# Performance work log

Measured on AMD Instinct MI355X. Metric: run time of the kernel, lower is better.

Reference implementation:

```python
import jax, jax.numpy as jnp
import numpy as np

N, M, K = 4, 50, 240000
POS_THRESH = 0.7
NEG_THRESH = 0.3
RPN_BATCH = 512
NUM_FG = RPN_BATCH // 2
NUM_BG = RPN_BATCH - NUM_FG
NEG_INF = -1e9


def setup_inputs() -> dict:
    key = jax.random.key(0)
    k1, k2, k3, k4, k5, k6 = jax.random.split(key, 6)
    # anchors: valid boxes (x1,y1,x2,y2) inside a ~960x600 image
    a_xy = jax.random.uniform(k1, (K, 2)) * jnp.array([900.0, 550.0])
    a_wh = jax.random.uniform(k2, (K, 2)) * 120.0 + 16.0
    anchors = jnp.concatenate([a_xy, a_xy + a_wh], axis=-1)
    g_xy = jax.random.uniform(k3, (N, M, 2)) * jnp.array([900.0, 550.0])
    g_wh = jax.random.uniform(k4, (N, M, 2)) * 120.0 + 16.0
    gt_boxes = jnp.concatenate([g_xy, g_xy + g_wh], axis=-1)
    rpn_cls_score = jax.random.normal(k5, (N, K))
    gt_labels = jax.random.randint(k6, (N, M), 1, 3, dtype=jnp.int32)
    return {"anchors": anchors, "rpn_cls_score": rpn_cls_score,
            "gt_boxes": gt_boxes, "gt_labels": gt_labels}


def _iou(anchors, gt_boxes):
    # anchors (K,4), gt_boxes (N,M,4) -> (N,K,M)
    a = anchors[None, :, None, :]   # (1,K,1,4)
    g = gt_boxes[:, None, :, :]     # (N,1,M,4)
    lt = jnp.maximum(a[..., :2], g[..., :2])
    rb = jnp.minimum(a[..., 2:], g[..., 2:])
    wh = jnp.clip(rb - lt, 0.0)
    inter = wh[..., 0] * wh[..., 1]
    area_a = (a[..., 2] - a[..., 0]) * (a[..., 3] - a[..., 1])
    area_g = (g[..., 2] - g[..., 0]) * (g[..., 3] - g[..., 1])
    return inter / (area_a + area_g - inter + 1e-8)


def _encode(anchors, matched):
    # anchors (K,4), matched (N,K,4) -> (N,K,4) standard (dx,dy,dw,dh)
    aw = anchors[:, 2] - anchors[:, 0]
    ah = anchors[:, 3] - anchors[:, 1]
    acx = anchors[:, 0] + 0.5 * aw
    acy = anchors[:, 1] + 0.5 * ah
    gw = matched[..., 2] - matched[..., 0]
    gh = matched[..., 3] - matched[..., 1]
    gcx = matched[..., 0] + 0.5 * gw
    gcy = matched[..., 1] + 0.5 * gh
    return jnp.stack([(gcx - acx) / aw, (gcy - acy) / ah,
                      jnp.log(gw / aw), jnp.log(gh / ah)], axis=-1)


def _subsample_one(score, pos, neg):
    # deterministic balanced sampler: top NUM_FG positives and top NUM_BG
    # negatives ranked by objectness criterion (hard mining)
    pos_key = jnp.where(pos, score, NEG_INF)
    neg_key = jnp.where(neg, score, NEG_INF)
    pv, pi = jax.lax.top_k(pos_key, NUM_FG)
    nv, ni = jax.lax.top_k(neg_key, NUM_BG)
    mask = jnp.zeros(score.shape[0], dtype=score.dtype)
    mask = mask.at[pi].max((pv > NEG_INF / 2).astype(score.dtype))
    mask = mask.at[ni].max((nv > NEG_INF / 2).astype(score.dtype))
    return mask


def reference(anchors, rpn_cls_score, gt_boxes, gt_labels):
    ious = _iou(anchors, gt_boxes)                 # (N,K,M)
    max_o = jnp.max(ious, axis=-1)                 # (N,K)
    argm = jnp.argmax(ious, axis=-1)               # (N,K)
    pos = max_o >= POS_THRESH
    neg = max_o < NEG_THRESH
    matched = jnp.take_along_axis(
        gt_boxes, jnp.broadcast_to(argm[:, :, None], (N, K, 4)), axis=1)
    matched_labels = jnp.take_along_axis(gt_labels, argm, axis=1)
    cls_targets = jnp.where(pos, matched_labels, 0)
    reg_targets = _encode(anchors, matched) * pos[..., None].astype(anchors.dtype)
    cls_weights = (pos | neg).astype(anchors.dtype)
    reg_weights = pos.astype(anchors.dtype)
    mask = jax.vmap(_subsample_one)(rpn_cls_score, pos, neg)  # (N,K)
    cls_weights = cls_weights * mask
    reg_weights = reg_weights * mask
    return cls_targets, reg_targets, cls_weights, reg_weights
```

## Files before the change

kernel.cpp:

```cpp
#include <hip/hip_runtime.h>

#define KA 240000
#define NI 4
#define MG 50
#define NSEL 256u
#define CAPL 4096
#define BPI 235
#define GRID (BPI * NI)
#define BPIK 469
#define GRIDK (BPIK * NI)

typedef unsigned int u32;

#define METAO 16384
#define LISTO (METAO + 32)
#define ONE_F 0x3F800000u

static __device__ __forceinline__ u32 sortkey32(float f) {
    u32 b = __float_as_uint(f);
    return (b & 0x80000000u) ? ~b : (b | 0x80000000u);
}
static __device__ __forceinline__ void patch1(u32* p) {
    __hip_atomic_store(p, ONE_F, __ATOMIC_RELAXED, __HIP_MEMORY_SCOPE_AGENT);
}

extern "C" __global__ void __launch_bounds__(256, 8)
AnchorTargetLayer_48052094107725_kernel(
    const float4* __restrict__ anchors, const float* __restrict__ scores,
    const float4* __restrict__ gtb, const int* __restrict__ glab,
    float* __restrict__ out, u32* __restrict__ flags, u32* __restrict__ ws) {
#pragma clang fp contract(off)
    __shared__ float4 gA[MG];
    __shared__ float gar[MG];
    __shared__ int glb[MG];
    __shared__ u32 lh[2048];
    const int bx = blockIdx.x;
    const int tid = threadIdx.x;
    const int n = bx / BPIK;
    const int kb = bx - n * BPIK;

    if (tid < 9) {
        const int i = bx * 9 + tid;
        if (i < LISTO) atomicExch(&ws[i], 0u);
    }
    for (int i = tid; i < 2048; i += 256) lh[i] = 0;
    if (tid < MG) {
        const float4 G = gtb[n * MG + tid];
        gA[tid] = G;
        gar[tid] = (G.z - G.x) * (G.w - G.y);
        glb[tid] = glab[n * MG + tid];
    }
    __syncthreads();

    const int k0 = (kb * 256 + tid) * 2;
    if (k0 < KA) {
        float ax0[2], ay0[2], ax2[2], ay2[2];
        #pragma unroll
        for (int j = 0; j < 2; ++j) {
            const float4 A = anchors[k0 + j];
            ax0[j] = A.x; ay0[j] = A.y; ax2[j] = A.z; ay2[j] = A.w;
        }
        float aaw[2], aah[2], aar[2];
        float biE[2], bSE[2], biO[2], bSO[2];
        int bixE[2], bixO[2];
        #pragma unroll
        for (int j = 0; j < 2; ++j) {
            aaw[j] = ax2[j] - ax0[j];
            aah[j] = ay2[j] - ay0[j];
            aar[j] = aaw[j] * aah[j];
            biE[j] = -1.0f; bSE[j] = 1.0f; bixE[j] = 0;
            biO[j] = -1.0f; bSO[j] = 1.0f; bixO[j] = 1;
        }
        #pragma unroll 5
        for (int m = 0; m < MG; m += 2) {
            const float4 Ga = gA[m];
            const float4 Gb = gA[m + 1];
            const float gaA = gar[m];
            const float gaB = gar[m + 1];
            #pragma unroll
            for (int j = 0; j < 2; ++j) {
                const float wa = fmaxf(fminf(ax2[j], Ga.z) - fmaxf(ax0[j], Ga.x), 0.0f);
                const float ha = fmaxf(fminf(ay2[j], Ga.w) - fmaxf(ay0[j], Ga.y), 0.0f);
                const float ia = wa * ha;
                const float sa = aar[j] + gaA;
                if (ia * bSE[j] > biE[j] * sa) { biE[j] = ia; bSE[j] = sa; bixE[j] = m; }
                const float wb = fmaxf(fminf(ax2[j], Gb.z) - fmaxf(ax0[j], Gb.x), 0.0f);
                const float hb = fmaxf(fminf(ay2[j], Gb.w) - fmaxf(ay0[j], Gb.y), 0.0f);
                const float ib = wb * hb;
                const float sb = aar[j] + gaB;
                if (ib * bSO[j] > biO[j] * sb) { biO[j] = ib; bSO[j] = sb; bixO[j] = m + 1; }
            }
        }

        const int nk = n * KA + k0;
        const float2 s2 = ((const float2*)scores)[nk >> 1];
        const float scv[2] = {s2.x, s2.y};

        float clsv[2];
        float4 regv[2];
        u32 flagpack = 0;
        #pragma unroll
        for (int j = 0; j < 2; ++j) {
            const float pO = biO[j] * bSE[j];
            const float pE = biE[j] * bSO[j];
            const bool takeO = (pO > pE) || (pO == pE && bixO[j] < bixE[j]);
            const float bi = takeO ? biO[j] : biE[j];
            const int  bix = takeO ? bixO[j] : bixE[j];
            const float da = ((aar[j] + gar[bix]) - bi) + 1e-8f;
            const float q = bi / da;
            const bool pos = q >= 0.7f;
            const bool neg = q < 0.3f;
            clsv[j] = pos ? (float)glb[bix] : 0.0f;
            float4 rv = make_float4(0.0f, 0.0f, 0.0f, 0.0f);
            if (pos) {
                const float4 Gm = gA[bix];
                const float gw = Gm.z - Gm.x, gh = Gm.w - Gm.y;
                const float gcx = Gm.x + 0.5f * gw, gcy = Gm.y + 0.5f * gh;
                const float acx = ax0[j] + 0.5f * aaw[j], acy = ay0[j] + 0.5f * aah[j];
                rv.x = (gcx - acx) / aaw[j];
                rv.y = (gcy - acy) / aah[j];
                rv.z = logf(gw / aaw[j]);
                rv.w = logf(gh / aah[j]);
            }
            regv[j] = rv;
            const u32 fl = pos ? 1u : (neg ? 2u : 0u);
            flagpack |= fl << (8 * j);
            if (fl) atomicAdd(&lh[sortkey32(scv[j]) >> 21], fl == 2u ? 0x10000u : 1u);
        }
        const size_t NK = (size_t)NI * KA;
        const int t2 = nk >> 1;
        ((float2*)out)[t2] = make_float2(clsv[0], clsv[1]);
        float4* regp = ((float4*)(out + NK)) + nk;
        regp[0] = regv[0]; regp[1] = regv[1];
        const float2 z2 = make_float2(0.0f, 0.0f);
        ((float2*)out)[(5 * NK >> 1) + t2] = z2;
        ((float2*)out)[(6 * NK >> 1) + t2] = z2;
        ((unsigned short*)flags)[t2] = (unsigned short)flagpack;
    }
    __syncthreads();
    const int gp = 2 * n;
    for (int i = tid; i < 2048; i += 256) {
        const u32 c = lh[i];
        if (c & 0xFFFFu) atomicAdd(&ws[gp * 2048 + i], c & 0xFFFFu);
        if (c >> 16)     atomicAdd(&ws[(gp + 1) * 2048 + i], c >> 16);
    }
}

__global__ void __launch_bounds__(256) kP(const float* __restrict__ scores,
                                          const u32* __restrict__ flagsW,
                                          u32* __restrict__ ws,
                                          float* __restrict__ out) {
    __shared__ u32 wsum[4];
    __shared__ u32 s_us[2], s_R[2], s_done[2];
    const int bx = blockIdx.x, tid = threadIdx.x;
    const int n = bx / BPI, kb = bx - n * BPI;
    const int lane = tid & 63, wv = tid >> 6;
    u32* hist = ws;
    u32* meta = ws + METAO;
    u32* list = ws + LISTO;

    for (int gi = 0; gi < 2; ++gi) {
        const int g = 2 * n + gi;
        u32 loc[8];
        u32 s = 0;
        const int base = g * 2048 + tid * 8;
        #pragma unroll
        for (int j = 0; j < 8; ++j) { loc[j] = hist[base + j]; s += loc[j]; }
        u32 v = s;
        #pragma unroll
        for (int d = 1; d < 64; d <<= 1) {
            const u32 t = __shfl_down(v, (unsigned)d, 64);
            v += (lane + d < 64) ? t : 0u;
        }
        if (lane == 0) wsum[wv] = v;
        __syncthreads();
        const u32 t0 = wsum[0], t1 = wsum[1], t2 = wsum[2], t3 = wsum[3];
        const u32 tot = t0 + t1 + t2 + t3;
        u32 above = 0;
        if (wv == 0) above = t1 + t2 + t3;
        else if (wv == 1) above = t2 + t3;
        else if (wv == 2) above = t3;
        v += above;
        if (tid == 0) s_done[gi] = (tot < NSEL) ? 1u : 0u;
        u32 run = v - s;
        #pragma unroll
        for (int j = 7; j >= 0; --j) {
            const u32 Sj = run + loc[j];
            if (Sj >= NSEL && run < NSEL) {
                s_us[gi] = (u32)(tid * 8 + j);
                s_R[gi] = NSEL - run;
            }
            run = Sj;
        }
        __syncthreads();
    }
    if (kb == 0 && tid == 0) {
        meta[2 * n] = s_us[0];     meta[8 + 2 * n] = s_R[0];     meta[16 + 2 * n] = s_done[0];
        meta[2 * n + 1] = s_us[1]; meta[8 + 2 * n + 1] = s_R[1]; meta[16 + 2 * n + 1] = s_done[1];
    }

    const int k0 = (kb * 256 + tid) * 4;
    if (k0 >= KA) return;
    const int nk = n * KA + k0;
    const u32 fw = flagsW[nk >> 2];
    if (!fw) return;
    const float4 s4 = ((const float4*)scores)[nk >> 2];
    const float scv[4] = {s4.x, s4.y, s4.z, s4.w};
    const size_t NK = (size_t)NI * KA;
    u32* o32 = (u32*)out;
    #pragma unroll
    for (int j = 0; j < 4; ++j) {
        const u32 f = (fw >> (8 * j)) & 255u;
        if (!f) continue;
        const int gi = (f == 2u) ? 1 : 0;
        bool in = false;
        if (s_done[gi]) {
            in = true;
        } else {
            const u32 key = sortkey32(scv[j]);
            const u32 p11 = key >> 21;
            if (p11 > s_us[gi]) {
                in = true;
            } else if (p11 == s_us[gi]) {
                const int g = 2 * n + gi;
                const u32 p = atomicAdd(&meta[24 + g], 1u);
                if (p < CAPL) {
                    list[(g * CAPL + p) * 2] = key;
                    list[(g * CAPL + p) * 2 + 1] = (u32)(k0 + j);
                }
            }
        }
        if (in) {
            patch1(&o32[5 * NK + nk + j]);
            if (f == 1u) patch1(&o32[6 * NK + nk + j]);
        }
    }
}

__global__ void __launch_bounds__(256) kR2(const u32* __restrict__ ws,
                                           float* __restrict__ out) {
    __shared__ u32 h2[1024];
    __shared__ u32 cs[256];
    __shared__ u32 s_usb, s_R2, s_tc;
    __shared__ u32 tk[256], ti[256];
    const u32* meta = ws + METAO;
    const u32* list = ws + LISTO;
    const int g = blockIdx.x, tid = threadIdx.x;
    if (meta[16 + g]) return;
    u32 c = meta[24 + g];
    if (c > CAPL) c = CAPL;
    const u32 R1 = meta[8 + g];
    for (u32 i = tid; i < 1024; i += 256) h2[i] = 0;
    if (tid == 0) s_tc = 0;
    __syncthreads();
    for (u32 j = tid; j < c; j += 256)
        atomicAdd(&h2[(list[(g * CAPL + j) * 2] >> 11) & 1023u], 1u);
    __syncthreads();
    u32 loc[4];
    u32 s = 0;
    #pragma unroll
    for (int j = 0; j < 4; ++j) { loc[j] = h2[tid * 4 + j]; s += loc[j]; }
    cs[tid] = s;
    __syncthreads();
    for (int d = 1; d < 256; d <<= 1) {
        const u32 add = (tid + d < 256) ? cs[tid + d] : 0u;
        __syncthreads();
        cs[tid] += add;
        __syncthreads();
    }
    u32 run = (tid < 255) ? cs[tid + 1] : 0u;
    #pragma unroll
    for (int j = 3; j >= 0; --j) {
        const u32 Sj = run + loc[j];
        if (Sj >= R1 && run < R1) { s_usb = (u32)(tid * 4 + j); s_R2 = R1 - run; }
        run = Sj;
    }
    __syncthreads();
    const u32 usb = s_usb, R2 = s_R2;
    const int nn = g >> 1;
    const bool posg = ((g & 1) == 0);
    const size_t NK = (size_t)NI * KA;
    u32* o32 = (u32*)out;
    for (u32 j = tid; j < c; j += 256) {
        const u32 key = list[(g * CAPL + j) * 2];
        const u32 idx = list[(g * CAPL + j) * 2 + 1];
        const u32 sb = (key >> 11) & 1023u;
        if (sb > usb) {
            const size_t o = (size_t)nn * KA + idx;
            patch1(&o32[5 * NK + o]);
            if (posg) patch1(&o32[6 * NK + o]);
        } else if (sb == usb) {
            const u32 p = atomicAdd(&s_tc, 1u);
            if (p < 256) { tk[p] = key; ti[p] = idx; }
        }
    }
    __syncthreads();
    u32 tc = s_tc;
    if (tc > 256) tc = 256;
    for (u32 i = tid; i < tc; i += 256) {
        const u32 ki = tk[i], ii = ti[i];
        u32 rank = 0;
        for (u32 j = 0; j < tc; ++j) {
            const u32 kj = tk[j];
            if (kj > ki || (kj == ki && ti[j] < ii)) rank++;
        }
        if (rank < R2) {
            const size_t o = (size_t)nn * KA + ii;
            patch1(&o32[5 * NK + o]);
            if (posg) patch1(&o32[6 * NK + o]);
        }
    }
}

extern "C" void kernel_launch(void* const* d_in, const int* in_sizes, int n_in,
                              void* d_out, int out_size, void* d_ws, size_t ws_size,
                              hipStream_t stream) {
    (void)in_sizes; (void)n_in; (void)out_size; (void)ws_size;
    const float4* anchors = (const float4*)d_in[0];
    const float*  scores  = (const float*)d_in[1];
    const float4* gtb     = (const float4*)d_in[2];
    const int*    glab    = (const int*)d_in[3];
    float* out = (float*)d_out;

    u32* ws = (u32*)d_ws;
    u32* flags = ws + LISTO + 8 * CAPL * 2;

    AnchorTargetLayer_48052094107725_kernel<<<GRIDK, 256, 0, stream>>>(
        anchors, scores, gtb, glab, out, flags, ws);
    kP<<<GRID, 256, 0, stream>>>(scores, flags, ws, out);
    kR2<<<8, 256, 0, stream>>>(ws, out);
}
```

Before: 126.0 us.

## Fuse final refinement pass into kP via last-block-done arrival counter

Removes the separate kR2 launch. Each kP block now bumps a per-image arrival counter after draining its memory writes, and the last block for an image runs the second-level radix refinement for both the positive and negative groups. This saves one kernel launch and its gap, but the refinement for each image now runs serially in a single block, and correctness depends on the counter being reset and on the atomic visibility ordering.

```diff
diff --git a/kernel.cpp b/kernel.cpp
--- a/kernel.cpp
+++ b/kernel.cpp
@@ -13,7 +13,8 @@
 typedef unsigned int u32;
 
 #define METAO 16384
-#define LISTO (METAO + 32)
+#define ARRO  (METAO + 32)
+#define LISTO (METAO + 40)
 #define ONE_F 0x3F800000u
 
 static __device__ __forceinline__ u32 sortkey32(float f) {
@@ -22,6 +23,15 @@
 }
 static __device__ __forceinline__ void patch1(u32* p) {
     __hip_atomic_store(p, ONE_F, __ATOMIC_RELAXED, __HIP_MEMORY_SCOPE_AGENT);
+}
+static __device__ __forceinline__ void astore(u32* p, u32 v) {
+    __hip_atomic_store(p, v, __ATOMIC_RELAXED, __HIP_MEMORY_SCOPE_AGENT);
+}
+static __device__ __forceinline__ u32 aload(const u32* p) {
+    return __hip_atomic_load(p, __ATOMIC_RELAXED, __HIP_MEMORY_SCOPE_AGENT);
+}
+static __device__ __forceinline__ void drain_vmem() {
+    asm volatile("s_waitcnt vmcnt(0)" ::: "memory");
 }
 
 extern "C" __global__ void __launch_bounds__(256, 8)
@@ -194,121 +204,124 @@
         }
         __syncthreads();
     }
-    if (kb == 0 && tid == 0) {
-        meta[2 * n] = s_us[0];     meta[8 + 2 * n] = s_R[0];     meta[16 + 2 * n] = s_done[0];
-        meta[2 * n + 1] = s_us[1]; meta[8 + 2 * n + 1] = s_R[1]; meta[16 + 2 * n + 1] = s_done[1];
-    }
-
-    const int k0 = (kb * 256 + tid) * 4;
-    if (k0 >= KA) return;
-    const int nk = n * KA + k0;
-    const u32 fw = flagsW[nk >> 2];
-    if (!fw) return;
-    const float4 s4 = ((const float4*)scores)[nk >> 2];
-    const float scv[4] = {s4.x, s4.y, s4.z, s4.w};
+
     const size_t NK = (size_t)NI * KA;
     u32* o32 = (u32*)out;
-    #pragma unroll
-    for (int j = 0; j < 4; ++j) {
-        const u32 f = (fw >> (8 * j)) & 255u;
-        if (!f) continue;
-        const int gi = (f == 2u) ? 1 : 0;
-        bool in = false;
-        if (s_done[gi]) {
-            in = true;
-        } else {
-            const u32 key = sortkey32(scv[j]);
-            const u32 p11 = key >> 21;
-            if (p11 > s_us[gi]) {
-                in = true;
-            } else if (p11 == s_us[gi]) {
-                const int g = 2 * n + gi;
-                const u32 p = atomicAdd(&meta[24 + g], 1u);
-                if (p < CAPL) {
-                    list[(g * CAPL + p) * 2] = key;
-                    list[(g * CAPL + p) * 2 + 1] = (u32)(k0 + j);
+
+    const int k0 = (kb * 256 + tid) * 4;
+    if (k0 < KA) {
+        const int nk = n * KA + k0;
+        const u32 fw = flagsW[nk >> 2];
+        if (fw) {
+            const float4 s4 = ((const float4*)scores)[nk >> 2];
+            const float scv[4] = {s4.x, s4.y, s4.z, s4.w};
+            #pragma unroll
+            for (int j = 0; j < 4; ++j) {
+                const u32 f = (fw >> (8 * j)) & 255u;
+                if (!f) continue;
+                const int gi = (f == 2u) ? 1 : 0;
+                bool in = false;
+                if (s_done[gi]) {
+                    in = true;
+                } else {
+                    const u32 key = sortkey32(scv[j]);
+                    const u32 p11 = key >> 21;
+                    if (p11 > s_us[gi]) {
+                        in = true;
+                    } else if (p11 == s_us[gi]) {
+                        const int g = 2 * n + gi;
+                        const u32 p = atomicAdd(&meta[24 + g], 1u);
+                        if (p < CAPL) {
+                            astore(&list[(g * CAPL + p) * 2], key);
+                            astore(&list[(g * CAPL + p) * 2 + 1], (u32)(k0 + j));
+                        }
+                    }
                 }
-            }
-        }
-        if (in) {
-            patch1(&o32[5 * NK + nk + j]);
-            if (f == 1u) patch1(&o32[6 * NK + nk + j]);
-        }
-    }
-}
-
-__global__ void __launch_bounds__(256) kR2(const u32* __restrict__ ws,
-                                           float* __restrict__ out) {
+                if (in) {
+                    patch1(&o32[5 * NK + nk + j]);
+                    if (f == 1u) patch1(&o32[6 * NK + nk + j]);
+                }
+            }
+        }
+    }
+
+    drain_vmem();
+    __syncthreads();
+    __shared__ u32 s_last;
+    if (tid == 0)
+        s_last = __hip_atomic_fetch_add(&ws[ARRO + n], 1u,
+                                        __ATOMIC_RELAXED, __HIP_MEMORY_SCOPE_AGENT);
+    __syncthreads();
+    if (s_last != BPI - 1) return;
+
     __shared__ u32 h2[1024];
     __shared__ u32 cs[256];
     __shared__ u32 s_usb, s_R2, s_tc;
     __shared__ u32 tk[256], ti[256];
-    const u32* meta = ws + METAO;
-    const u32* list = ws + LISTO;
-    const int g = blockIdx.x, tid = threadIdx.x;
-    if (meta[16 + g]) return;
-    u32 c = meta[24 + g];
-    if (c > CAPL) c = CAPL;
-    const u32 R1 = meta[8 + g];
-    for (u32 i = tid; i < 1024; i += 256) h2[i] = 0;
-    if (tid == 0) s_tc = 0;
-    __syncthreads();
-    for (u32 j = tid; j < c; j += 256)
-        atomicAdd(&h2[(list[(g * CAPL + j) * 2] >> 11) & 1023u], 1u);
-    __syncthreads();
-    u32 loc[4];
-    u32 s = 0;
-    #pragma unroll
-    for (int j = 0; j < 4; ++j) { loc[j] = h2[tid * 4 + j]; s += loc[j]; }
-    cs[tid] = s;
-    __syncthreads();
-    for (int d = 1; d < 256; d <<= 1) {
-        const u32 add = (tid + d < 256) ? cs[tid + d] : 0u;
-        __syncthreads();
-        cs[tid] += add;
-        __syncthreads();
-    }
-    u32 run = (tid < 255) ? cs[tid + 1] : 0u;
-    #pragma unroll
-    for (int j = 3; j >= 0; --j) {
-        const u32 Sj = run + loc[j];
-        if (Sj >= R1 && run < R1) { s_usb = (u32)(tid * 4 + j); s_R2 = R1 - run; }
-        run = Sj;
-    }
-    __syncthreads();
-    const u32 usb = s_usb, R2 = s_R2;
-    const int nn = g >> 1;
-    const bool posg = ((g & 1) == 0);
-    const size_t NK = (size_t)NI * KA;
-    u32* o32 = (u32*)out;
-    for (u32 j = tid; j < c; j += 256) {
-        const u32 key = list[(g * CAPL + j) * 2];
-        const u32 idx = list[(g * CAPL + j) * 2 + 1];
-        const u32 sb = (key >> 11) & 1023u;
-        if (sb > usb) {
-            const size_t o = (size_t)nn * KA + idx;
-            patch1(&o32[5 * NK + o]);
-            if (posg) patch1(&o32[6 * NK + o]);
-        } else if (sb == usb) {
-            const u32 p = atomicAdd(&s_tc, 1u);
-            if (p < 256) { tk[p] = key; ti[p] = idx; }
-        }
-    }
-    __syncthreads();
-    u32 tc = s_tc;
-    if (tc > 256) tc = 256;
-    for (u32 i = tid; i < tc; i += 256) {
-        const u32 ki = tk[i], ii = ti[i];
-        u32 rank = 0;
-        for (u32 j = 0; j < tc; ++j) {
-            const u32 kj = tk[j];
-            if (kj > ki || (kj == ki && ti[j] < ii)) rank++;
-        }
-        if (rank < R2) {
-            const size_t o = (size_t)nn * KA + ii;
-            patch1(&o32[5 * NK + o]);
-            if (posg) patch1(&o32[6 * NK + o]);
-        }
+    for (int gi = 0; gi < 2; ++gi) {
+        if (s_done[gi]) continue;
+        const int g = 2 * n + gi;
+        u32 c = aload(&meta[24 + g]);
+        if (c > CAPL) c = CAPL;
+        const u32 R1 = s_R[gi];
+        for (u32 i = tid; i < 1024; i += 256) h2[i] = 0;
+        if (tid == 0) s_tc = 0;
+        __syncthreads();
+        for (u32 j = tid; j < c; j += 256)
+            atomicAdd(&h2[(aload(&list[(g * CAPL + j) * 2]) >> 11) & 1023u], 1u);
+        __syncthreads();
+        u32 loc[4];
+        u32 s = 0;
+        #pragma unroll
+        for (int j = 0; j < 4; ++j) { loc[j] = h2[tid * 4 + j]; s += loc[j]; }
+        cs[tid] = s;
+        __syncthreads();
+        for (int d = 1; d < 256; d <<= 1) {
+            const u32 add = (tid + d < 256) ? cs[tid + d] : 0u;
+            __syncthreads();
+            cs[tid] += add;
+            __syncthreads();
+        }
+        u32 run = (tid < 255) ? cs[tid + 1] : 0u;
+        #pragma unroll
+        for (int j = 3; j >= 0; --j) {
+            const u32 Sj = run + loc[j];
+            if (Sj >= R1 && run < R1) { s_usb = (u32)(tid * 4 + j); s_R2 = R1 - run; }
+            run = Sj;
+        }
+        __syncthreads();
+        const u32 usb = s_usb, R2 = s_R2;
+        const bool posg = (gi == 0);
+        for (u32 j = tid; j < c; j += 256) {
+            const u32 key = aload(&list[(g * CAPL + j) * 2]);
+            const u32 idx = aload(&list[(g * CAPL + j) * 2 + 1]);
+            const u32 sb = (key >> 11) & 1023u;
+            if (sb > usb) {
+                const size_t o = (size_t)n * KA + idx;
+                patch1(&o32[5 * NK + o]);
+                if (posg) patch1(&o32[6 * NK + o]);
+            } else if (sb == usb) {
+                const u32 p = atomicAdd(&s_tc, 1u);
+                if (p < 256) { tk[p] = key; ti[p] = idx; }
+            }
+        }
+        __syncthreads();
+        u32 tc = s_tc;
+        if (tc > 256) tc = 256;
+        for (u32 i = tid; i < tc; i += 256) {
+            const u32 ki = tk[i], ii = ti[i];
+            u32 rank = 0;
+            for (u32 j2 = 0; j2 < tc; ++j2) {
+                const u32 kj = tk[j2];
+                if (kj > ki || (kj == ki && ti[j2] < ii)) rank++;
+            }
+            if (rank < R2) {
+                const size_t o = (size_t)n * KA + ii;
+                patch1(&o32[5 * NK + o]);
+                if (posg) patch1(&o32[6 * NK + o]);
+            }
+        }
+        __syncthreads();
     }
 }
 
@@ -328,5 +341,4 @@
     AnchorTargetLayer_48052094107725_kernel<<<GRIDK, 256, 0, stream>>>(
         anchors, scores, gtb, glab, out, flags, ws);
     kP<<<GRID, 256, 0, stream>>>(scores, flags, ws, out);
-    kR2<<<8, 256, 0, stream>>>(ws, out);
-}
+}
```

Measured after the change: 130.3 us. 3.4% more time.
